# Performance work log

Measured on AMD Instinct MI355X. Metric: run time of the kernel, lower is better.

## Reference

```python
import jax, jax.numpy as jnp
import numpy as np

B, S, D = 32, 512, 512
GH, LH = 8, 4            # global / local num_heads
W, STRIDE = 10, 5        # local window size and hop (window_size // 2)


def _mha(x, w_in, b_in, w_out, b_out, n_heads, key_mask=None):
    """Torch nn.MultiheadAttention (self-attn, eval mode). x: [N, L, D]."""
    N, L, d = x.shape
    dh = d // n_heads
    qkv = x @ w_in.T + b_in                       # [N, L, 3D]
    q, k, v = jnp.split(qkv, 3, axis=-1)
    def heads(t):
        return t.reshape(N, L, n_heads, dh).transpose(0, 2, 1, 3)  # [N,H,L,dh]
    q, k, v = heads(q), heads(k), heads(v)
    scores = jnp.einsum('bhqd,bhkd->bhqk', q, k) / jnp.sqrt(jnp.asarray(dh, x.dtype))
    if key_mask is not None:                      # key_mask: [N, L] bool, True = valid
        scores = jnp.where(key_mask[:, None, None, :], scores, jnp.asarray(-1e9, x.dtype))
    attn = jax.nn.softmax(scores, axis=-1)
    out = jnp.einsum('bhqk,bhkd->bhqd', attn, v).transpose(0, 2, 1, 3).reshape(N, L, d)
    return out @ w_out.T + b_out


def setup_inputs() -> dict:
    key = jax.random.key(0)
    ks = jax.random.split(key, 12)
    s = 0.02
    return {
        'x':      jax.random.normal(ks[0], (B, S, D), jnp.float32),
        'gw_in':  jax.random.normal(ks[1], (3 * D, D), jnp.float32) * s,
        'gb_in':  jnp.zeros((3 * D,), jnp.float32),
        'gw_out': jax.random.normal(ks[2], (D, D), jnp.float32) * s,
        'gb_out': jnp.zeros((D,), jnp.float32),
        'lw_in':  jax.random.normal(ks[3], (3 * D, D), jnp.float32) * s,
        'lb_in':  jnp.zeros((3 * D,), jnp.float32),
        'lw_out': jax.random.normal(ks[4], (D, D), jnp.float32) * s,
        'lb_out': jnp.zeros((D,), jnp.float32),
        'fw':     jax.random.normal(ks[5], (D, 2 * D), jnp.float32) * s,
        'fb':     jnp.zeros((D,), jnp.float32),
    }


def reference(x, gw_in, gb_in, gw_out, gb_out, lw_in, lb_in, lw_out, lb_out, fw, fb):
    # ---- global branch: full self-attention over the sequence ----
    global_out = _mha(x, gw_in, gb_in, gw_out, gb_out, GH)

    # ---- local branch: overlapping windows of size W, hop STRIDE ----
    starts = np.arange(0, S, STRIDE)              # static window starts
    NW = len(starts)
    pos = starts[:, None] + np.arange(W)          # [NW, W] absolute positions
    valid = pos < S                               # ragged tail windows
    idx = np.minimum(pos, S - 1)                  # clipped gather indices

    windows = x[:, idx]                           # [B, NW, W, D]
    windows = windows.reshape(B * NW, W, D)
    key_mask = jnp.broadcast_to(jnp.asarray(valid)[None], (B, NW, W)).reshape(B * NW, W)

    local_attn = _mha(windows, lw_in, lb_in, lw_out, lb_out, LH, key_mask=key_mask)
    local_attn = local_attn.reshape(B, NW, W, D) * jnp.asarray(valid)[None, :, :, None].astype(x.dtype)

    # scatter-add overlapping window outputs back (matches `local_out[:, i:end] +=`)
    local_out = jnp.zeros_like(x).at[:, idx.reshape(-1)].add(local_attn.reshape(B, NW * W, D))

    # ---- fusion MLP (dropout = identity in eval) ----
    combined = jnp.concatenate([global_out, local_out], axis=-1)   # [B, S, 2D]
    return jax.nn.relu(combined @ fw.T + fb)
```

## Files before the change

kernel.cpp:

```cpp
#include <hip/hip_runtime.h>
#include <cstdint>
#include <cstddef>

#define DEV __device__ __forceinline__

typedef float f32x4 __attribute__((ext_vector_type(4)));
typedef short bf16x8 __attribute__((ext_vector_type(8)));

DEV unsigned short f2bf(float f) {
  union { float f; unsigned u; } v; v.f = f;
  unsigned u = v.u;
  unsigned r = u + 0x7FFFu + ((u >> 16) & 1u);
  return (unsigned short)(r >> 16);
}
DEV float bf2f(unsigned short h) {
  union { unsigned u; float f; } v; v.u = ((unsigned)h) << 16;
  return v.f;
}
DEV unsigned cvtpk(float lo, float hi) {
  unsigned r;
  asm("v_cvt_pk_bf16_f32 %0, %1, %2" : "=v"(r) : "v"(lo), "v"(hi));
  return r;
}

DEV void gload16(const void* g, void* l) {
  __builtin_amdgcn_global_load_lds((const __attribute__((address_space(1))) unsigned int*)g,
                                   (__attribute__((address_space(3))) unsigned int*)l,
                                   16, 0, 0);
}

DEV f32x4 MFMA(bf16x8 a, bf16x8 b, f32x4 c) {
  return __builtin_amdgcn_mfma_f32_16x16x32_bf16(a, b, c, 0, 0, 0);
}

__global__ void k_f2bf(const float* __restrict__ src, unsigned short* __restrict__ dst, int n) {
  int i = (blockIdx.x * blockDim.x + threadIdx.x) * 4;
  int stride = gridDim.x * blockDim.x * 4;
  for (; i < n; i += stride) {
    float4 v = *(const float4*)(src + i);
    ushort4 o;
    o.x = f2bf(v.x); o.y = f2bf(v.y); o.z = f2bf(v.z); o.w = f2bf(v.w);
    *(ushort4*)(dst + i) = o;
  }
}

__global__ __launch_bounds__(256) void k_merge(const float* __restrict__ fw,
                                               const float* __restrict__ gw_out,
                                               const float* __restrict__ lw_out,
                                               unsigned short* __restrict__ M1b,
                                               unsigned short* __restrict__ M2b) {
  __shared__ float Fa[64][68];
  __shared__ float Gb[64][68];
  const int bi = blockIdx.x, bj = blockIdx.y, m2 = blockIdx.z;
  const float* g = m2 ? lw_out : gw_out;
  const int i0 = bi * 64, j0 = bj * 64;
  const int tid = threadIdx.x;
  const int tr = tid >> 4, tc = tid & 15;
  float acc[4][4] = {};
  for (int kc = 0; kc < 8; kc++) {
    int k0 = kc * 64;
    __syncthreads();
    #pragma unroll
    for (int it = 0; it < 4; it++) {
      int r = tr + 16 * it;
      float4 v = *(const float4*)(fw + (size_t)(i0 + r) * 1024 + m2 * 512 + k0 + tc * 4);
      Fa[tc * 4 + 0][r] = v.x; Fa[tc * 4 + 1][r] = v.y;
      Fa[tc * 4 + 2][r] = v.z; Fa[tc * 4 + 3][r] = v.w;
      *(float4*)&Gb[r][tc * 4] = *(const float4*)(g + (size_t)(k0 + r) * 512 + j0 + tc * 4);
    }
    __syncthreads();
    for (int k = 0; k < 64; k++) {
      float4 a4 = *(const float4*)&Fa[k][tr * 4];
      float4 b4 = *(const float4*)&Gb[k][tc * 4];
      float av[4] = {a4.x, a4.y, a4.z, a4.w};
      float bv[4] = {b4.x, b4.y, b4.z, b4.w};
      #pragma unroll
      for (int r = 0; r < 4; r++)
        #pragma unroll
        for (int c = 0; c < 4; c++)
          acc[r][c] += av[r] * bv[c];
    }
  }
  unsigned short* M = m2 ? M2b : M1b;
  #pragma unroll
  for (int r = 0; r < 4; r++) {
    ushort4 pk;
    pk.x = f2bf(acc[r][0]); pk.y = f2bf(acc[r][1]);
    pk.z = f2bf(acc[r][2]); pk.w = f2bf(acc[r][3]);
    *(ushort4*)&M[(size_t)(i0 + tr * 4 + r) * 512 + j0 + tc * 4] = pk;
  }
}

__global__ __launch_bounds__(256) void k_bias(const float* __restrict__ fw, const float* __restrict__ gb_out,
                                              const float* __restrict__ lb_out, const float* __restrict__ fb,
                                              float* __restrict__ bias1, float* __restrict__ bias2) {
  __shared__ float bv[512];
  const int which = blockIdx.y;
  const int i0 = blockIdx.x * 64;
  const float* src = which ? lb_out : gb_out;
  for (int t = threadIdx.x; t < 512; t += 256) bv[t] = src[t];
  __syncthreads();
  const int r = threadIdx.x >> 2, c4 = threadIdx.x & 3;
  const float* frow = fw + (size_t)(i0 + r) * 1024 + (which ? 512 : 0) + c4 * 128;
  float a = 0.f;
  #pragma unroll 4
  for (int k = 0; k < 128; k += 4) {
    float4 v = *(const float4*)(frow + k);
    a += v.x * bv[c4 * 128 + k] + v.y * bv[c4 * 128 + k + 1]
       + v.z * bv[c4 * 128 + k + 2] + v.w * bv[c4 * 128 + k + 3];
  }
  a += __shfl_xor(a, 1);
  a += __shfl_xor(a, 2);
  if (c4 == 0) {
    int i = i0 + r;
    if (which) bias2[i] = a;
    else       bias1[i] = a + fb[i];
  }
}

template <int EPI>
__global__ __launch_bounds__(256) void k_gemm(const unsigned short* __restrict__ A,
                                              const unsigned short* __restrict__ A2,
                                              const unsigned short* __restrict__ Wm,
                                              const unsigned short* __restrict__ W2,
                                              const float* __restrict__ bias,
                                              const float* __restrict__ bias2,
                                              float qscale, void* __restrict__ Cout,
                                              int Ntot, int NT) {
  __shared__ unsigned short As[2][128 * 32];
  __shared__ unsigned short Bs[2][128 * 32];
  const int tid = threadIdx.x;
  const int wave = tid >> 6, lane = tid & 63;
  const int wr = wave >> 1, wc = wave & 1;
  const int bm = blockIdx.x, bn = blockIdx.y;
  const int ql = lane & 15, kg = lane >> 4;

  const int c0 = wave * 2;
  const int srow = lane >> 2;
  const int sks = (lane & 3) * 8;

  auto stage = [&](int buf, int t) {
    const unsigned short* sA = A;
    const unsigned short* sW = Wm;
    int k0 = t * 32;
    if (EPI == 1 && t >= 16) { sA = A2; sW = W2; k0 = (t - 16) * 32; }
    #pragma unroll
    for (int i = 0; i < 2; i++) {
      int c = c0 + i;
      int row = c * 16 + srow;
      gload16(sA + (size_t)(bm * 128 + row) * 512 + k0 + sks, &As[buf][c * 512 + lane * 8]);
      gload16(sW + (size_t)(bn * 128 + row) * 512 + k0 + sks, &Bs[buf][c * 512 + lane * 8]);
    }
  };

  f32x4 acc[4][4] = {};
  stage(0, 0);
  __syncthreads();
  for (int t = 0; t < NT; t++) {
    int buf = t & 1;
    if (t + 1 < NT) stage(buf ^ 1, t + 1);
    const unsigned short* as = As[buf];
    const unsigned short* bs = Bs[buf];
    bf16x8 af[4], bfr[4];
    #pragma unroll
    for (int m = 0; m < 4; m++)
      af[m] = *(const bf16x8*)&as[(wr * 64 + m * 16 + ql) * 32 + kg * 8];
    #pragma unroll
    for (int n = 0; n < 4; n++)
      bfr[n] = *(const bf16x8*)&bs[(wc * 64 + n * 16 + ql) * 32 + kg * 8];
    #pragma unroll
    for (int m = 0; m < 4; m++)
      #pragma unroll
      for (int n = 0; n < 4; n++)
        acc[m][n] = MFMA(af[m], bfr[n], acc[m][n]);
    __syncthreads();
  }

  const int row0 = bm * 128 + wr * 64;
  const int col0 = bn * 128 + wc * 64;
  if (EPI == 0) {
    unsigned short* C = (unsigned short*)Cout;
    #pragma unroll
    for (int m = 0; m < 4; m++)
      #pragma unroll
      for (int n = 0; n < 4; n++) {
        int col = col0 + n * 16 + ql;
        float bcol = bias[col];
        float qs = (col < 512) ? qscale : 1.0f;
        #pragma unroll
        for (int r = 0; r < 4; r++) {
          int row = row0 + m * 16 + kg * 4 + r;
          C[(size_t)row * Ntot + col] = f2bf((acc[m][n][r] + bcol) * qs);
        }
      }
  } else {
    float* C = (float*)Cout;
    #pragma unroll
    for (int m = 0; m < 4; m++)
      #pragma unroll
      for (int n = 0; n < 4; n++) {
        int col = col0 + n * 16 + ql;
        float b1 = bias[col], b2 = bias2[col];
        #pragma unroll
        for (int r = 0; r < 4; r++) {
          int row = row0 + m * 16 + kg * 4 + r;
          float cc = ((row & 511) < 5) ? 1.0f : 2.0f;
          float v = acc[m][n][r] + b1 + cc * b2;
          C[(size_t)row * 512 + col] = fmaxf(v, 0.0f);
        }
      }
  }
}

__global__ __launch_bounds__(512, 2) void k_attn_g(const unsigned short* __restrict__ QKV,
                                                   unsigned short* __restrict__ Og) {
  __shared__ unsigned short Klds[512 * 64];
  __shared__ unsigned short Vt[64 * 512];
  __shared__ unsigned short Plds[8][16 * 64];
  const int tid = threadIdx.x, wave = tid >> 6, lane = tid & 63;
  const int ql = lane & 15, kg = lane >> 4;
  const int h = blockIdx.x, b = blockIdx.y;
  const size_t tb = (size_t)b * 512;
  const size_t hoff = (size_t)h * 64;

  #pragma unroll
  for (int i = 0; i < 8; i++) {
    int instr = wave * 8 + i;
    int row = instr * 8 + (lane >> 3);
    int slot = lane & 7;
    int c = slot ^ (row & 7);
    gload16(QKV + (tb + row) * 1536 + 512 + hoff + c * 8, &Klds[instr * 512 + lane * 8]);
  }
  {
    const unsigned short* Vp = QKV + (tb + tid) * 1536 + 1024 + hoff;
    const int kc = tid >> 3, ke = tid & 7;
    #pragma unroll
    for (int c8 = 0; c8 < 8; c8++) {
      bf16x8 v8 = *(const bf16x8*)(Vp + c8 * 8);
      #pragma unroll
      for (int j = 0; j < 8; j++) {
        int d = c8 * 8 + j;
        Vt[d * 512 + (((kc ^ (d & 7)) << 3) | ke)] = (unsigned short)v8[j];
      }
    }
  }
  bf16x8 qf[4][2];
  #pragma unroll
  for (int m = 0; m < 4; m++) {
    const unsigned short* Qp = QKV + (tb + wave * 64 + m * 16 + ql) * 1536 + hoff;
    qf[m][0] = *(const bf16x8*)(Qp + kg * 8);
    qf[m][1] = *(const bf16x8*)(Qp + 32 + kg * 8);
  }
  __syncthreads();

  float l_part[4] = {};
  f32x4 o[4][4] = {};
  unsigned short* Pw = &Plds[wave][0];
  const int pswz = 2 * (ql & 7);

  for (int kv = 0; kv < 8; kv++) {
    const int k0 = kv * 64;
    bf16x8 kf[4][2], vb[4][2];
    #pragma unroll
    for (int f = 0; f < 4; f++) {
      int row = k0 + 16 * f + ql;
      #pragma unroll
      for (int c = 0; c < 2; c++)
        kf[f][c] = *(const bf16x8*)&Klds[row * 64 + (((c * 4 + kg) ^ (row & 7)) * 8)];
      #pragma unroll
      for (int st = 0; st < 2; st++) {
        int d = 16 * f + ql;
        int ch = (k0 >> 3) + st * 4 + kg;
        vb[f][st] = *(const bf16x8*)&Vt[d * 512 + ((ch ^ (d & 7)) * 8)];
      }
    }
    #pragma unroll
    for (int m = 0; m < 4; m++) {
      f32x4 s[4] = {};
      #pragma unroll
      for (int f = 0; f < 4; f++) {
        s[f] = MFMA(kf[f][0], qf[m][0], s[f]);
        s[f] = MFMA(kf[f][1], qf[m][1], s[f]);
      }
      #pragma unroll
      for (int f = 0; f < 4; f++) {
        #pragma unroll
        for (int r = 0; r < 4; r++)
          s[f][r] = exp2f(s[f][r]);
        l_part[m] += (s[f][0] + s[f][1]) + (s[f][2] + s[f][3]);
        uint2 pk;
        pk.x = cvtpk(s[f][0], s[f][1]);
        pk.y = cvtpk(s[f][2], s[f][3]);
        *(uint2*)&Pw[ql * 64 + (((4 * f + kg) ^ pswz) * 4)] = pk;
      }
      #pragma unroll
      for (int st = 0; st < 2; st++) {
        bf16x8 pa = *(const bf16x8*)&Pw[ql * 64 + (((8 * st + 2 * kg) ^ pswz) * 4)];
        #pragma unroll
        for (int f = 0; f < 4; f++)
          o[m][f] = MFMA(pa, vb[f][st], o[m][f]);
      }
    }
  }

  #pragma unroll
  for (int m = 0; m < 4; m++) {
    float l = l_part[m];
    l += __shfl_xor(l, 16);
    l += __shfl_xor(l, 32);
    #pragma unroll
    for (int r = 0; r < 4; r++) {
      float inv = 1.0f / __shfl(l, kg * 4 + r);
      size_t row = tb + wave * 64 + m * 16 + kg * 4 + r;
      #pragma unroll
      for (int f = 0; f < 4; f++)
        Og[row * 512 + hoff + 16 * f + ql] = f2bf(o[m][f][r] * inv);
    }
  }
}

__global__ __launch_bounds__(256) void k_attn_l(const unsigned short* __restrict__ QKV,
                                                unsigned short* __restrict__ Lacc) {
  __shared__ unsigned short Qs[5][520];
  __shared__ unsigned short Ks[15][520];
  __shared__ unsigned short Vs[15][520];
  __shared__ float Pb[2][4][5][13];
  const int w = blockIdx.x, b = blockIdx.y;
  const int p0 = 5 * w;
  const int tid = threadIdx.x;
  const size_t tbase = (size_t)b * 512;

  for (int c = tid; c < 35 * 64; c += 256) {
    int row = c >> 6, ch = (c & 63) * 8;
    if (row < 5) {
      int tok = min(p0 + row, 511);
      *(bf16x8*)&Qs[row][ch] = *(const bf16x8*)(QKV + (tbase + tok) * 1536 + ch);
    } else if (row < 20) {
      int rr = row - 5;
      int tok = min(max(p0 - 5 + rr, 0), 511);
      *(bf16x8*)&Ks[rr][ch] = *(const bf16x8*)(QKV + (tbase + tok) * 1536 + 512 + ch);
    } else {
      int rr = row - 20;
      int tok = min(max(p0 - 5 + rr, 0), 511);
      *(bf16x8*)&Vs[rr][ch] = *(const bf16x8*)(QKV + (tbase + tok) * 1536 + 1024 + ch);
    }
  }
  __syncthreads();

  #pragma unroll
  for (int rep = 0; rep < 2; rep++) {
    int idx = tid + rep * 256;
    if (idx < 400) {
      int j = idx % 10;
      int t1 = idx / 10;
      int q = t1 % 5;
      int t2 = t1 / 5;
      int h = t2 & 3;
      int win = t2 >> 2;
      int krow = win ? j : j + 5;
      int ktok = p0 - 5 + krow;
      float scv = -1e30f;
      bool ok = (win == 0 || w > 0) && (p0 + q < 512) && (ktok < 512);
      if (ok) {
        float acc = 0.f;
        const unsigned short* qp = &Qs[q][h * 128];
        const unsigned short* kp = &Ks[krow][h * 128];
        #pragma unroll
        for (int ck = 0; ck < 16; ck++) {
          bf16x8 q8 = *(const bf16x8*)(qp + ck * 8);
          bf16x8 k8 = *(const bf16x8*)(kp + ck * 8);
          #pragma unroll
          for (int e = 0; e < 8; e++)
            acc += bf2f((unsigned short)q8[e]) * bf2f((unsigned short)k8[e]);
        }
        scv = acc;
      }
      Pb[win][h][q][j] = scv;
    }
  }
  __syncthreads();

  if (tid < 40) {
    int q = tid % 5;
    int t2 = tid / 5;
    int h = t2 & 3;
    int win = t2 >> 2;
    float* row = &Pb[win][h][q][0];
    float mx = -1e30f;
    #pragma unroll
    for (int j = 0; j < 10; j++) mx = fmaxf(mx, row[j]);
    float e[10]; float su = 0.f;
    #pragma unroll
    for (int j = 0; j < 10; j++) {
      float v = row[j];
      float ej = (v <= -1e29f) ? 0.f : exp2f(v - mx);
      e[j] = ej; su += ej;
    }
    float inv = (su > 0.f) ? 1.0f / su : 0.f;
    #pragma unroll
    for (int j = 0; j < 10; j++) row[j] = e[j] * inv;
  }
  __syncthreads();

  {
    const int h = tid >> 6;
    const int d = tid * 2;
    for (int qq = 0; qq < 5; qq++) {
      int p = p0 + qq;
      if (p >= 512) break;
      float a0 = 0.f, a1 = 0.f;
      const float* P0 = &Pb[0][h][qq][0];
      #pragma unroll
      for (int j = 0; j < 10; j++) {
        float pw = P0[j];
        a0 += pw * bf2f(Vs[j + 5][d]);
        a1 += pw * bf2f(Vs[j + 5][d + 1]);
      }
      if (w > 0) {
        const float* P1 = &Pb[1][h][qq][0];
        #pragma unroll
        for (int j = 0; j < 10; j++) {
          float pw = P1[j];
          a0 += pw * bf2f(Vs[j][d]);
          a1 += pw * bf2f(Vs[j][d + 1]);
        }
      }
      ushort2 st; st.x = f2bf(a0); st.y = f2bf(a1);
      *(ushort2*)&Lacc[(tbase + p) * 512 + d] = st;
    }
  }
}

extern "C" void kernel_launch(void* const* d_in, const int* in_sizes, int n_in,
                              void* d_out, int out_size, void* d_ws, size_t ws_size,
                              hipStream_t stream) {
  const float* x      = (const float*)d_in[0];
  const float* gw_in  = (const float*)d_in[1];
  const float* gb_in  = (const float*)d_in[2];
  const float* gw_out = (const float*)d_in[3];
  const float* gb_out = (const float*)d_in[4];
  const float* lw_in  = (const float*)d_in[5];
  const float* lb_in  = (const float*)d_in[6];
  const float* lw_out = (const float*)d_in[7];
  const float* lb_out = (const float*)d_in[8];
  const float* fw     = (const float*)d_in[9];
  const float* fb     = (const float*)d_in[10];

  char* ws = (char*)d_ws;
  auto alloc = [&](size_t bytes) -> char* {
    char* p = ws;
    ws += (bytes + 255) & ~(size_t)255;
    return p;
  };
  unsigned short* xb     = (unsigned short*)alloc((size_t)16384 * 512 * 2);
  unsigned short* gwin_b = (unsigned short*)alloc((size_t)1536 * 512 * 2);
  unsigned short* lwin_b = (unsigned short*)alloc((size_t)1536 * 512 * 2);
  unsigned short* M1b    = (unsigned short*)alloc((size_t)512 * 512 * 2);
  unsigned short* M2b    = (unsigned short*)alloc((size_t)512 * 512 * 2);
  float* bias1           = (float*)alloc(512 * 4);
  float* bias2           = (float*)alloc(512 * 4);
  unsigned short* QKV    = (unsigned short*)alloc((size_t)16384 * 1536 * 2);
  unsigned short* Og     = (unsigned short*)alloc((size_t)16384 * 512 * 2);
  unsigned short* La     = (unsigned short*)alloc((size_t)16384 * 512 * 2);

  k_f2bf<<<2048, 256, 0, stream>>>(x, xb, 16384 * 512);
  k_f2bf<<<128, 256, 0, stream>>>(gw_in, gwin_b, 1536 * 512);
  k_f2bf<<<128, 256, 0, stream>>>(lw_in, lwin_b, 1536 * 512);
  k_merge<<<dim3(8, 8, 2), 256, 0, stream>>>(fw, gw_out, lw_out, M1b, M2b);
  k_bias<<<dim3(8, 2), 256, 0, stream>>>(fw, gb_out, lb_out, fb, bias1, bias2);

  k_gemm<0><<<dim3(128, 12), 256, 0, stream>>>(xb, nullptr, gwin_b, nullptr, gb_in, nullptr,
                                               0.125f * 1.44269504f, QKV, 1536, 16);
  k_attn_g<<<dim3(8, 32), 512, 0, stream>>>(QKV, Og);

  k_gemm<0><<<dim3(128, 12), 256, 0, stream>>>(xb, nullptr, lwin_b, nullptr, lb_in, nullptr,
                                               0.08838834764831845f * 1.44269504f, QKV, 1536, 16);
  k_attn_l<<<dim3(103, 32), 256, 0, stream>>>(QKV, La);

  k_gemm<1><<<dim3(128, 4), 256, 0, stream>>>(Og, La, M1b, M2b, bias1, bias2,
                                              1.0f, d_out, 512, 32);
}
```

Measured before the change: 220.9 us.

## Keep attention probabilities in registers by computing transposed PV product

The global attention kernel no longer round-trips the exponentiated scores through a per-wave LDS buffer. It computes O^T = V^T·P^T, feeding the S accumulator registers directly as the B operand after packing them to bf16. To make that work, the V tile is stored in a permuted, padded layout whose key order matches the MFMA accumulator lane layout. The output store then writes four contiguous bf16 values per lane, and the row sum no longer needs a shuffle to normalise. This removes LDS writes and reads plus a wave-local dependency per tile, at the cost of a trickier V permutation and a different LDS padding pattern that may change bank conflicts.

```diff
diff --git a/kernel.cpp b/kernel.cpp
--- a/kernel.cpp
+++ b/kernel.cpp
@@ -215,8 +215,7 @@
 __global__ __launch_bounds__(512, 2) void k_attn_g(const unsigned short* __restrict__ QKV,
                                                    unsigned short* __restrict__ Og) {
   __shared__ unsigned short Klds[512 * 64];
-  __shared__ unsigned short Vt[64 * 512];
-  __shared__ unsigned short Plds[8][16 * 64];
+  __shared__ unsigned short Vt[64][536];
   const int tid = threadIdx.x, wave = tid >> 6, lane = tid & 63;
   const int ql = lane & 15, kg = lane >> 4;
   const int h = blockIdx.x, b = blockIdx.y;
@@ -232,16 +231,15 @@
     gload16(QKV + (tb + row) * 1536 + 512 + hoff + c * 8, &Klds[instr * 512 + lane * 8]);
   }
   {
+    int k64 = tid & 63;
+    int f = k64 >> 4, kgv = (k64 >> 2) & 3, r = k64 & 3;
+    int sig = (tid & ~63) + 32 * (f >> 1) + 4 * (f & 1) + 8 * kgv + r;
     const unsigned short* Vp = QKV + (tb + tid) * 1536 + 1024 + hoff;
-    const int kc = tid >> 3, ke = tid & 7;
     #pragma unroll
     for (int c8 = 0; c8 < 8; c8++) {
       bf16x8 v8 = *(const bf16x8*)(Vp + c8 * 8);
       #pragma unroll
-      for (int j = 0; j < 8; j++) {
-        int d = c8 * 8 + j;
-        Vt[d * 512 + (((kc ^ (d & 7)) << 3) | ke)] = (unsigned short)v8[j];
-      }
+      for (int j = 0; j < 8; j++) Vt[c8 * 8 + j][sig] = (unsigned short)v8[j];
     }
   }
   bf16x8 qf[4][2];
@@ -254,9 +252,7 @@
   __syncthreads();
 
   float l_part[4] = {};
-  f32x4 o[4][4] = {};
-  unsigned short* Pw = &Plds[wave][0];
-  const int pswz = 2 * (ql & 7);
+  f32x4 ot[4][4] = {};
 
   for (int kv = 0; kv < 8; kv++) {
     const int k0 = kv * 64;
@@ -268,11 +264,8 @@
       for (int c = 0; c < 2; c++)
         kf[f][c] = *(const bf16x8*)&Klds[row * 64 + (((c * 4 + kg) ^ (row & 7)) * 8)];
       #pragma unroll
-      for (int st = 0; st < 2; st++) {
-        int d = 16 * f + ql;
-        int ch = (k0 >> 3) + st * 4 + kg;
-        vb[f][st] = *(const bf16x8*)&Vt[d * 512 + ((ch ^ (d & 7)) * 8)];
-      }
+      for (int st = 0; st < 2; st++)
+        vb[f][st] = *(const bf16x8*)&Vt[16 * f + ql][k0 + st * 32 + kg * 8];
     }
     #pragma unroll
     for (int m = 0; m < 4; m++) {
@@ -288,17 +281,18 @@
         for (int r = 0; r < 4; r++)
           s[f][r] = exp2f(s[f][r]);
         l_part[m] += (s[f][0] + s[f][1]) + (s[f][2] + s[f][3]);
-        uint2 pk;
-        pk.x = cvtpk(s[f][0], s[f][1]);
-        pk.y = cvtpk(s[f][2], s[f][3]);
-        *(uint2*)&Pw[ql * 64 + (((4 * f + kg) ^ pswz) * 4)] = pk;
       }
       #pragma unroll
       for (int st = 0; st < 2; st++) {
-        bf16x8 pa = *(const bf16x8*)&Pw[ql * 64 + (((8 * st + 2 * kg) ^ pswz) * 4)];
-        #pragma unroll
-        for (int f = 0; f < 4; f++)
-          o[m][f] = MFMA(pa, vb[f][st], o[m][f]);
+        union { unsigned w[4]; bf16x8 v; } pb;
+        #pragma unroll
+        for (int w = 0; w < 4; w++) {
+          int f = 2 * st + (w >> 1);
+          pb.w[w] = cvtpk(s[f][2 * (w & 1)], s[f][2 * (w & 1) + 1]);
+        }
+        #pragma unroll
+        for (int fp = 0; fp < 4; fp++)
+          ot[m][fp] = MFMA(vb[fp][st], pb.v, ot[m][fp]);
       }
     }
   }
@@ -308,13 +302,16 @@
     float l = l_part[m];
     l += __shfl_xor(l, 16);
     l += __shfl_xor(l, 32);
-    #pragma unroll
-    for (int r = 0; r < 4; r++) {
-      float inv = 1.0f / __shfl(l, kg * 4 + r);
-      size_t row = tb + wave * 64 + m * 16 + kg * 4 + r;
-      #pragma unroll
-      for (int f = 0; f < 4; f++)
-        Og[row * 512 + hoff + 16 * f + ql] = f2bf(o[m][f][r] * inv);
+    float inv = 1.0f / l;
+    size_t row = tb + wave * 64 + m * 16 + ql;
+    #pragma unroll
+    for (int fp = 0; fp < 4; fp++) {
+      ushort4 st4;
+      st4.x = f2bf(ot[m][fp][0] * inv);
+      st4.y = f2bf(ot[m][fp][1] * inv);
+      st4.z = f2bf(ot[m][fp][2] * inv);
+      st4.w = f2bf(ot[m][fp][3] * inv);
+      *(ushort4*)&Og[row * 512 + hoff + 16 * fp + 4 * kg] = st4;
     }
   }
 }
```

New measurement: 220.0 us. Within noise of the previous version (-0.4%).
